# Kernel tuning notes

Hardware: AMD Instinct MI355X
Metric: run time of the kernel (lower is better)

The kernel has to match this reference:

```python
import jax, jax.numpy as jnp
import numpy as np
from jax import lax

N, M, T, V, C_IN, C_OUT, KT, PAD = 16, 2, 300, 25, 64, 64, 9, 4
BN_EPS = 1e-5

# NTU-RGB+D 25-joint skeleton edges (0-indexed), symmetric, plus self-loops
_NTU_EDGES = [(0,1),(1,20),(2,20),(3,2),(4,20),(5,4),(6,5),(7,6),(8,20),(9,8),
              (10,9),(11,10),(12,0),(13,12),(14,13),(15,14),(16,0),(17,16),
              (18,17),(19,18),(21,22),(22,7),(23,24),(24,11)]

def _build_adj():
    A = np.zeros((V, V), dtype=np.float32)
    for i, j in _NTU_EDGES:
        A[i, j] = 1.0
        A[j, i] = 1.0
    A += np.eye(V, dtype=np.float32)  # self-loops (DGL GCN preprocessing)
    return jnp.asarray(A)


def setup_inputs() -> dict:
    key = jax.random.key(0)
    ks = jax.random.split(key, 8)
    stdv = 1.0 / np.sqrt(C_OUT)
    # conv_init: normal(0, sqrt(2/(out_channels*prod(kernel))))
    conv_std = np.sqrt(2.0 / (C_OUT * KT * 1))
    return {
        "h": jax.random.normal(ks[0], (N * M * T * V, C_IN), dtype=jnp.float32),
        "adj": _build_adj(),
        "gcn_w": jax.random.uniform(ks[1], (C_IN, C_OUT), minval=-stdv, maxval=stdv, dtype=jnp.float32),
        "gcn_b": jax.random.uniform(ks[2], (C_OUT,), minval=-stdv, maxval=stdv, dtype=jnp.float32),
        "conv_w": conv_std * jax.random.normal(ks[3], (C_OUT, C_OUT, KT, 1), dtype=jnp.float32),
        "conv_b": jnp.zeros((C_OUT,), dtype=jnp.float32),
        "bn_gamma": jnp.ones((C_OUT,), dtype=jnp.float32),
        "bn_beta": jnp.zeros((C_OUT,), dtype=jnp.float32),
        "bn_mean": 0.1 * jax.random.normal(ks[4], (C_OUT,), dtype=jnp.float32),
        "bn_var": jax.random.uniform(ks[5], (C_OUT,), minval=0.5, maxval=1.5, dtype=jnp.float32),
    }


def reference(h, adj, gcn_w, gcn_b, conv_w, conv_b, bn_gamma, bn_beta, bn_mean, bn_var):
    # ---- GCNLayer (dropout is identity at eval) ----
    # symmetric norm = deg^{-1/2}, identical across the N*M*T copies of the skeleton
    norm = adj.sum(axis=1) ** -0.5                      # (V,)
    x = h @ gcn_w                                        # (N*M*T*V, C_OUT)
    x = x.reshape(-1, V, C_OUT) * norm[:, None]          # pre-norm scale
    x = jnp.einsum('vu,buc->bvc', adj, x)                # copy_src + sum aggregation
    x = x * norm[:, None] + gcn_b                        # post-norm scale + bias
    x = jax.nn.relu(x)

    # ---- TemporalConvNetwork ----
    v = x.reshape(N, M, T, V, C_OUT)
    v = v.transpose(0, 1, 4, 2, 3).reshape(N * M, C_OUT, T, V)   # (NM, C, T, V)
    v = lax.conv_general_dilated(v, conv_w, window_strides=(1, 1),
                                 padding=[(PAD, PAD), (0, 0)],
                                 dimension_numbers=('NCHW', 'OIHW', 'NCHW'))
    v = v + conv_b[None, :, None, None]
    inv_std = bn_gamma / jnp.sqrt(bn_var + BN_EPS)       # eval-mode BatchNorm2d
    v = (v - bn_mean[None, :, None, None]) * inv_std[None, :, None, None] + bn_beta[None, :, None, None]
    v = jax.nn.relu(v)
    v = v.reshape(N, M, C_OUT, T, V).transpose(0, 1, 3, 4, 2)    # (N, M, T, V, C)

    # ---- residual (downt is None since in_feats == out_feats and stride == 1) ----
    return v + h.reshape(N, M, T, V, C_IN)
```

## Files before the change

kernel.cpp:

```cpp
#include <hip/hip_runtime.h>
#include <hip/hip_bf16.h>


typedef __bf16 bf16x8 __attribute__((ext_vector_type(8)));
typedef __bf16 bf16x4 __attribute__((ext_vector_type(4)));
typedef float  f32x4  __attribute__((ext_vector_type(4)));

#define Y_OFF   0
#define WC2_OFF 30720000
#define WGT_OFF 30793728
#define A2P_OFF 30801920
#define SC_OFF  30803968
#define SH_OFF  30804224

__global__ __launch_bounds__(256) void prep_kernel(
    const float* __restrict__ adj, const float* __restrict__ gcn_w,
    const float* __restrict__ conv_w, const float* __restrict__ conv_b,
    const float* __restrict__ bn_g, const float* __restrict__ bn_b,
    const float* __restrict__ bn_m, const float* __restrict__ bn_v,
    __bf16* __restrict__ wc2, __bf16* __restrict__ wgt,
    __bf16* __restrict__ a2p, float* __restrict__ scale, float* __restrict__ shift) {
  int tid = threadIdx.x;
  for (int e = blockIdx.x * 256 + tid; e < 36864; e += gridDim.x * 256) {
    int j = e & 7, t1 = e >> 3, c = t1 & 63, g = t1 >> 6;
    int kap = g * 8 + j, kt = kap >> 6, ci = kap & 63;
    wc2[e] = (__bf16)conv_w[(c * 64 + ci) * 9 + kt];
  }
  if (blockIdx.x == 0) {
    for (int e = tid; e < 4096; e += 256) {
      int c = e >> 6, k = e & 63;
      wgt[e] = (__bf16)gcn_w[k * 64 + c];
    }
  } else if (blockIdx.x == 1) {
    for (int e = tid; e < 1024; e += 256) {
      int v = e >> 5, u = e & 31;
      float val = 0.f;
      if (v < 25 && u < 25) {
        float dv = 0.f, du = 0.f;
        for (int t = 0; t < 25; ++t) { dv += adj[v * 25 + t]; du += adj[u * 25 + t]; }
        val = rsqrtf(dv) * adj[v * 25 + u] * rsqrtf(du);
      }
      a2p[e] = (__bf16)val;
    }
  } else if (blockIdx.x == 2) {
    if (tid < 64) {
      float sc = bn_g[tid] * rsqrtf(bn_v[tid] + 1e-5f);
      scale[tid] = sc;
      shift[tid] = (conv_b[tid] - bn_m[tid]) * sc + bn_b[tid];
    }
  }
}

__global__ __launch_bounds__(256, 4) void gcn_kernel(
    const float* __restrict__ h, const __bf16* __restrict__ wgt_g,
    const __bf16* __restrict__ a2p_g, const float* __restrict__ gcn_b,
    __bf16* __restrict__ y) {
  __shared__ __align__(16) __bf16 hb[4][2048];
  __shared__ __align__(16) __bf16 x1t[4][2048];
  int tid = threadIdx.x, w = tid >> 6, lane = tid & 63;
  int l15 = lane & 15, quad = lane >> 4;
  int skel = blockIdx.x * 4 + w;
  int nm = skel / 300, tloc = skel - nm * 300;

  bf16x8 awg[4][2];
  for (int mt = 0; mt < 4; ++mt)
    for (int kk = 0; kk < 2; ++kk)
      awg[mt][kk] = *(const bf16x8*)&wgt_g[(mt * 16 + l15) * 64 + kk * 32 + quad * 8];
  bf16x8 ba[2];
  for (int nt = 0; nt < 2; ++nt)
    ba[nt] = *(const bf16x8*)&a2p_g[(nt * 16 + l15) * 32 + quad * 8];

  if (lane < 56) *(uint4*)&hb[w][1600 + lane * 8] = (uint4){0u, 0u, 0u, 0u};
  for (int it = 0; it < 7; ++it) {
    int u = it * 4 + quad;
    if (u < 25) {
      float4 hv = *(const float4*)&h[(skel * 25 + u) * 64 + l15 * 4];
      bf16x4 b4; b4[0] = (__bf16)hv.x; b4[1] = (__bf16)hv.y; b4[2] = (__bf16)hv.z; b4[3] = (__bf16)hv.w;
      int ch = l15 >> 1;
      *(bf16x4*)&hb[w][u * 64 + (((ch ^ (u & 7)) * 8) | ((l15 & 1) * 4))] = b4;
    }
  }
  for (int mt = 0; mt < 4; ++mt)
    for (int nt = 0; nt < 2; ++nt) {
      f32x4 acc = {0.f, 0.f, 0.f, 0.f};
      int u = nt * 16 + l15;
      for (int kk = 0; kk < 2; ++kk) {
        bf16x8 b = *(const bf16x8*)&hb[w][u * 64 + (((kk * 4 + quad) ^ (u & 7)) * 8)];
        acc = __builtin_amdgcn_mfma_f32_16x16x32_bf16(awg[mt][kk], b, acc, 0, 0, 0);
      }
      int c0 = mt * 16 + quad * 4;
      for (int r = 0; r < 4; ++r) x1t[w][(c0 + r) * 32 + u] = (__bf16)acc[r];
    }
  for (int mt = 0; mt < 4; ++mt)
    for (int nt = 0; nt < 2; ++nt) {
      f32x4 acc = {0.f, 0.f, 0.f, 0.f};
      bf16x8 a = *(const bf16x8*)&x1t[w][(mt * 16 + l15) * 32 + quad * 8];
      acc = __builtin_amdgcn_mfma_f32_16x16x32_bf16(a, ba[nt], acc, 0, 0, 0);
      int v = nt * 16 + l15, c0 = mt * 16 + quad * 4;
      if (v < 25) {
        float4 bias = *(const float4*)&gcn_b[c0];
        bf16x4 o;
        o[0] = (__bf16)fmaxf(acc[0] + bias.x, 0.f);
        o[1] = (__bf16)fmaxf(acc[1] + bias.y, 0.f);
        o[2] = (__bf16)fmaxf(acc[2] + bias.z, 0.f);
        o[3] = (__bf16)fmaxf(acc[3] + bias.w, 0.f);
        int ch = (c0 >> 3) ^ (v & 7);
        *(bf16x4*)&hb[w][v * 64 + ((ch * 8) | (c0 & 7))] = o;
      }
    }
  for (int e = lane; e < 200; e += 64) {
    int v = e >> 3, ch = e & 7;
    uint4 val = *(const uint4*)&hb[w][v * 64 + ((ch ^ (v & 7)) * 8)];
    *(uint4*)&y[((nm * 25 + v) * 300 + tloc) * 64 + ch * 8] = val;
  }
}

__global__ __launch_bounds__(64, 4) void conv_kernel(
    const __bf16* __restrict__ y, const __bf16* __restrict__ wc2,
    const float* __restrict__ scale, const float* __restrict__ shift,
    const float* __restrict__ h, float* __restrict__ out) {
  __shared__ __align__(16) __bf16 my[72 * 64];
  int lane = threadIdx.x;
  int l15 = lane & 15, quad = lane >> 4;
  int gid = blockIdx.x;
  int ti = gid % 5, r1 = gid / 5;
  int vv = r1 % 25, nm = r1 / 25;
  int t0 = (ti < 4) ? ti * 64 : 236;

  {
    const __bf16* ybase = &y[((nm * 25 + vv) * 300) * 64];
    uint4 stg[9];
    for (int it = 0; it < 9; ++it) {
      int idx = it * 64 + lane, r = idx >> 3, ch = idx & 7;
      int tg = t0 - 4 + r;
      uint4 val = {0u, 0u, 0u, 0u};
      if (tg >= 0 && tg < 300) val = *(const uint4*)&ybase[tg * 64 + ch * 8];
      stg[it] = val;
    }
    for (int it = 0; it < 9; ++it) {
      int idx = it * 64 + lane, r = idx >> 3, ch = idx & 7;
      *(uint4*)&my[r * 64 + ((ch ^ (r & 7)) * 8)] = stg[it];
    }
  }

  f32x4 acc[4][4];
  for (int m = 0; m < 4; ++m) for (int n = 0; n < 4; ++n) acc[m][n] = (f32x4){0.f, 0.f, 0.f, 0.f};

  bf16x8 a0[4], a1[4];
#define LOADA(dst, kk_) { const __bf16* wb = wc2 + (((kk_) * 4 + quad) * 64) * 8; \
    for (int m = 0; m < 4; ++m) dst[m] = *(const bf16x8*)&wb[(m * 16 + l15) * 8]; }
#define COMPUTE(kk_, areg) { int kt = (kk_) >> 1, chb = ((kk_) & 1) * 4 + quad; \
    for (int n = 0; n < 4; ++n) { \
      int row = n * 16 + l15 + kt; \
      bf16x8 b = *(const bf16x8*)&my[row * 64 + ((chb ^ (row & 7)) * 8)]; \
      for (int m = 0; m < 4; ++m) \
        acc[m][n] = __builtin_amdgcn_mfma_f32_16x16x32_bf16(areg[m], b, acc[m][n], 0, 0, 0); \
    } }
  LOADA(a0, 0)
  for (int kk = 0; kk < 18; kk += 2) {
    LOADA(a1, kk + 1)
    COMPUTE(kk, a0)
    if (kk + 2 < 18) LOADA(a0, kk + 2)
    COMPUTE(kk + 1, a1)
  }
#undef LOADA
#undef COMPUTE

  for (int n = 0; n < 4; ++n) {
    int tt = t0 + n * 16 + l15;
    for (int m = 0; m < 4; ++m) {
      int c0 = m * 16 + quad * 4;
      int idx = ((nm * 300 + tt) * 25 + vv) * 64 + c0;
      float4 sc = *(const float4*)&scale[c0];
      float4 sh = *(const float4*)&shift[c0];
      float4 hr = *(const float4*)&h[idx];
      float4 o;
      o.x = fmaxf(acc[m][n][0] * sc.x + sh.x, 0.f) + hr.x;
      o.y = fmaxf(acc[m][n][1] * sc.y + sh.y, 0.f) + hr.y;
      o.z = fmaxf(acc[m][n][2] * sc.z + sh.z, 0.f) + hr.z;
      o.w = fmaxf(acc[m][n][3] * sc.w + sh.w, 0.f) + hr.w;
      *(float4*)&out[idx] = o;
    }
  }
}

extern "C" void kernel_launch(void* const* d_in, const int* in_sizes, int n_in,
                              void* d_out, int out_size, void* d_ws, size_t ws_size,
                              hipStream_t stream) {
  const float* h      = (const float*)d_in[0];
  const float* adj    = (const float*)d_in[1];
  const float* gcn_w  = (const float*)d_in[2];
  const float* gcn_b  = (const float*)d_in[3];
  const float* conv_w = (const float*)d_in[4];
  const float* conv_b = (const float*)d_in[5];
  const float* bn_g   = (const float*)d_in[6];
  const float* bn_b   = (const float*)d_in[7];
  const float* bn_m   = (const float*)d_in[8];
  const float* bn_v   = (const float*)d_in[9];
  float* out = (float*)d_out;
  char* ws = (char*)d_ws;

  __bf16* y_ws   = (__bf16*)(ws + Y_OFF);
  __bf16* wc2    = (__bf16*)(ws + WC2_OFF);
  __bf16* wgt    = (__bf16*)(ws + WGT_OFF);
  __bf16* a2p    = (__bf16*)(ws + A2P_OFF);
  float*  scale  = (float*)(ws + SC_OFF);
  float*  shift  = (float*)(ws + SH_OFF);

  prep_kernel<<<64, 256, 0, stream>>>(adj, gcn_w, conv_w, conv_b, bn_g, bn_b, bn_m, bn_v,
                                      wc2, wgt, a2p, scale, shift);
  gcn_kernel<<<2400, 256, 0, stream>>>(h, wgt, a2p, gcn_b, y_ws);
  conv_kernel<<<4000, 64, 0, stream>>>(y_ws, wc2, scale, shift, h, out);
}
```

Baseline: 174.2 us.

## Split conv output channels across four waves; one-wave gcn blocks with padded LDS

The conv kernel now runs 256-thread blocks in which each of the four waves computes 16 output channels over the shared 72-row tile, instead of one wave computing all 64 channels. This cuts accumulator registers and raises occupancy and wave count, at the cost of a __syncthreads and the input tile being loaded once per block by more threads. The gcn kernel moves from four skeletons per 256-thread block to one skeleton per 64-thread block, and pads the transposed intermediate row stride from 32 to 40 to reduce LDS bank conflicts. The conv grid becomes a 3D dim3 launch, which removes the index divisions.

```diff
diff --git a/kernel.cpp b/kernel.cpp
--- a/kernel.cpp
+++ b/kernel.cpp
@@ -51,15 +51,15 @@
   }
 }
 
-__global__ __launch_bounds__(256, 4) void gcn_kernel(
+__global__ __launch_bounds__(64) void gcn_kernel(
     const float* __restrict__ h, const __bf16* __restrict__ wgt_g,
     const __bf16* __restrict__ a2p_g, const float* __restrict__ gcn_b,
     __bf16* __restrict__ y) {
-  __shared__ __align__(16) __bf16 hb[4][2048];
-  __shared__ __align__(16) __bf16 x1t[4][2048];
-  int tid = threadIdx.x, w = tid >> 6, lane = tid & 63;
+  __shared__ __align__(16) __bf16 hb[2048];
+  __shared__ __align__(16) __bf16 x1t[64 * 40];
+  int lane = threadIdx.x;
   int l15 = lane & 15, quad = lane >> 4;
-  int skel = blockIdx.x * 4 + w;
+  int skel = blockIdx.x;
   int nm = skel / 300, tloc = skel - nm * 300;
 
   bf16x8 awg[4][2];
@@ -70,14 +70,14 @@
   for (int nt = 0; nt < 2; ++nt)
     ba[nt] = *(const bf16x8*)&a2p_g[(nt * 16 + l15) * 32 + quad * 8];
 
-  if (lane < 56) *(uint4*)&hb[w][1600 + lane * 8] = (uint4){0u, 0u, 0u, 0u};
+  if (lane < 56) *(uint4*)&hb[1600 + lane * 8] = (uint4){0u, 0u, 0u, 0u};
   for (int it = 0; it < 7; ++it) {
     int u = it * 4 + quad;
     if (u < 25) {
       float4 hv = *(const float4*)&h[(skel * 25 + u) * 64 + l15 * 4];
       bf16x4 b4; b4[0] = (__bf16)hv.x; b4[1] = (__bf16)hv.y; b4[2] = (__bf16)hv.z; b4[3] = (__bf16)hv.w;
       int ch = l15 >> 1;
-      *(bf16x4*)&hb[w][u * 64 + (((ch ^ (u & 7)) * 8) | ((l15 & 1) * 4))] = b4;
+      *(bf16x4*)&hb[u * 64 + (((ch ^ (u & 7)) * 8) | ((l15 & 1) * 4))] = b4;
     }
   }
   for (int mt = 0; mt < 4; ++mt)
@@ -85,16 +85,16 @@
       f32x4 acc = {0.f, 0.f, 0.f, 0.f};
       int u = nt * 16 + l15;
       for (int kk = 0; kk < 2; ++kk) {
-        bf16x8 b = *(const bf16x8*)&hb[w][u * 64 + (((kk * 4 + quad) ^ (u & 7)) * 8)];
+        bf16x8 b = *(const bf16x8*)&hb[u * 64 + (((kk * 4 + quad) ^ (u & 7)) * 8)];
         acc = __builtin_amdgcn_mfma_f32_16x16x32_bf16(awg[mt][kk], b, acc, 0, 0, 0);
       }
       int c0 = mt * 16 + quad * 4;
-      for (int r = 0; r < 4; ++r) x1t[w][(c0 + r) * 32 + u] = (__bf16)acc[r];
+      for (int r = 0; r < 4; ++r) x1t[(c0 + r) * 40 + u] = (__bf16)acc[r];
     }
   for (int mt = 0; mt < 4; ++mt)
     for (int nt = 0; nt < 2; ++nt) {
       f32x4 acc = {0.f, 0.f, 0.f, 0.f};
-      bf16x8 a = *(const bf16x8*)&x1t[w][(mt * 16 + l15) * 32 + quad * 8];
+      bf16x8 a = *(const bf16x8*)&x1t[(mt * 16 + l15) * 40 + quad * 8];
       acc = __builtin_amdgcn_mfma_f32_16x16x32_bf16(a, ba[nt], acc, 0, 0, 0);
       int v = nt * 16 + l15, c0 = mt * 16 + quad * 4;
       if (v < 25) {
@@ -105,56 +105,58 @@
         o[2] = (__bf16)fmaxf(acc[2] + bias.z, 0.f);
         o[3] = (__bf16)fmaxf(acc[3] + bias.w, 0.f);
         int ch = (c0 >> 3) ^ (v & 7);
-        *(bf16x4*)&hb[w][v * 64 + ((ch * 8) | (c0 & 7))] = o;
+        *(bf16x4*)&hb[v * 64 + ((ch * 8) | (c0 & 7))] = o;
       }
     }
   for (int e = lane; e < 200; e += 64) {
     int v = e >> 3, ch = e & 7;
-    uint4 val = *(const uint4*)&hb[w][v * 64 + ((ch ^ (v & 7)) * 8)];
+    uint4 val = *(const uint4*)&hb[v * 64 + ((ch ^ (v & 7)) * 8)];
     *(uint4*)&y[((nm * 25 + v) * 300 + tloc) * 64 + ch * 8] = val;
   }
 }
 
-__global__ __launch_bounds__(64, 4) void conv_kernel(
+__global__ __launch_bounds__(256, 8) void conv_kernel(
     const __bf16* __restrict__ y, const __bf16* __restrict__ wc2,
     const float* __restrict__ scale, const float* __restrict__ shift,
     const float* __restrict__ h, float* __restrict__ out) {
   __shared__ __align__(16) __bf16 my[72 * 64];
-  int lane = threadIdx.x;
+  int tid = threadIdx.x, w = tid >> 6, lane = tid & 63;
   int l15 = lane & 15, quad = lane >> 4;
-  int gid = blockIdx.x;
-  int ti = gid % 5, r1 = gid / 5;
-  int vv = r1 % 25, nm = r1 / 25;
+  int ti = blockIdx.x, vv = blockIdx.y, nm = blockIdx.z;
   int t0 = (ti < 4) ? ti * 64 : 236;
 
   {
     const __bf16* ybase = &y[((nm * 25 + vv) * 300) * 64];
-    uint4 stg[9];
-    for (int it = 0; it < 9; ++it) {
-      int idx = it * 64 + lane, r = idx >> 3, ch = idx & 7;
-      int tg = t0 - 4 + r;
+    uint4 stg[3];
+    for (int it = 0; it < 3; ++it) {
+      int idx = it * 256 + tid;
       uint4 val = {0u, 0u, 0u, 0u};
-      if (tg >= 0 && tg < 300) val = *(const uint4*)&ybase[tg * 64 + ch * 8];
+      if (idx < 576) {
+        int r = idx >> 3, ch = idx & 7, tg = t0 - 4 + r;
+        if (tg >= 0 && tg < 300) val = *(const uint4*)&ybase[tg * 64 + ch * 8];
+      }
       stg[it] = val;
     }
-    for (int it = 0; it < 9; ++it) {
-      int idx = it * 64 + lane, r = idx >> 3, ch = idx & 7;
-      *(uint4*)&my[r * 64 + ((ch ^ (r & 7)) * 8)] = stg[it];
-    }
-  }
-
-  f32x4 acc[4][4];
-  for (int m = 0; m < 4; ++m) for (int n = 0; n < 4; ++n) acc[m][n] = (f32x4){0.f, 0.f, 0.f, 0.f};
-
-  bf16x8 a0[4], a1[4];
-#define LOADA(dst, kk_) { const __bf16* wb = wc2 + (((kk_) * 4 + quad) * 64) * 8; \
-    for (int m = 0; m < 4; ++m) dst[m] = *(const bf16x8*)&wb[(m * 16 + l15) * 8]; }
+    for (int it = 0; it < 3; ++it) {
+      int idx = it * 256 + tid;
+      if (idx < 576) {
+        int r = idx >> 3, ch = idx & 7;
+        *(uint4*)&my[r * 64 + ((ch ^ (r & 7)) * 8)] = stg[it];
+      }
+    }
+  }
+  __syncthreads();
+
+  f32x4 acc[4];
+  for (int n = 0; n < 4; ++n) acc[n] = (f32x4){0.f, 0.f, 0.f, 0.f};
+
+  bf16x8 a0, a1;
+#define LOADA(dst, kk_) dst = *(const bf16x8*)&wc2[((((kk_) * 4 + quad) * 64) + w * 16 + l15) * 8];
 #define COMPUTE(kk_, areg) { int kt = (kk_) >> 1, chb = ((kk_) & 1) * 4 + quad; \
     for (int n = 0; n < 4; ++n) { \
       int row = n * 16 + l15 + kt; \
       bf16x8 b = *(const bf16x8*)&my[row * 64 + ((chb ^ (row & 7)) * 8)]; \
-      for (int m = 0; m < 4; ++m) \
-        acc[m][n] = __builtin_amdgcn_mfma_f32_16x16x32_bf16(areg[m], b, acc[m][n], 0, 0, 0); \
+      acc[n] = __builtin_amdgcn_mfma_f32_16x16x32_bf16(areg, b, acc[n], 0, 0, 0); \
     } }
   LOADA(a0, 0)
   for (int kk = 0; kk < 18; kk += 2) {
@@ -166,21 +168,19 @@
 #undef LOADA
 #undef COMPUTE
 
+  int c0 = w * 16 + quad * 4;
+  float4 sc = *(const float4*)&scale[c0];
+  float4 sh = *(const float4*)&shift[c0];
   for (int n = 0; n < 4; ++n) {
     int tt = t0 + n * 16 + l15;
-    for (int m = 0; m < 4; ++m) {
-      int c0 = m * 16 + quad * 4;
-      int idx = ((nm * 300 + tt) * 25 + vv) * 64 + c0;
-      float4 sc = *(const float4*)&scale[c0];
-      float4 sh = *(const float4*)&shift[c0];
-      float4 hr = *(const float4*)&h[idx];
-      float4 o;
-      o.x = fmaxf(acc[m][n][0] * sc.x + sh.x, 0.f) + hr.x;
-      o.y = fmaxf(acc[m][n][1] * sc.y + sh.y, 0.f) + hr.y;
-      o.z = fmaxf(acc[m][n][2] * sc.z + sh.z, 0.f) + hr.z;
-      o.w = fmaxf(acc[m][n][3] * sc.w + sh.w, 0.f) + hr.w;
-      *(float4*)&out[idx] = o;
-    }
+    int idx = ((nm * 300 + tt) * 25 + vv) * 64 + c0;
+    float4 hr = *(const float4*)&h[idx];
+    float4 o;
+    o.x = fmaxf(acc[n][0] * sc.x + sh.x, 0.f) + hr.x;
+    o.y = fmaxf(acc[n][1] * sc.y + sh.y, 0.f) + hr.y;
+    o.z = fmaxf(acc[n][2] * sc.z + sh.z, 0.f) + hr.z;
+    o.w = fmaxf(acc[n][3] * sc.w + sh.w, 0.f) + hr.w;
+    *(float4*)&out[idx] = o;
   }
 }
 
@@ -209,6 +209,6 @@
 
   prep_kernel<<<64, 256, 0, stream>>>(adj, gcn_w, conv_w, conv_b, bn_g, bn_b, bn_m, bn_v,
                                       wc2, wgt, a2p, scale, shift);
-  gcn_kernel<<<2400, 256, 0, stream>>>(h, wgt, a2p, gcn_b, y_ws);
-  conv_kernel<<<4000, 64, 0, stream>>>(y_ws, wc2, scale, shift, h, out);
-}
+  gcn_kernel<<<9600, 64, 0, stream>>>(h, wgt, a2p, gcn_b, y_ws);
+  conv_kernel<<<dim3(5, 25, 32), 256, 0, stream>>>(y_ws, wc2, scale, shift, h, out);
+}
```

New measurement: 170.0 us. -2.4%, faster.
